# Kernel tuning notes

Measured on AMD Instinct MI355X. Metric: run time of the kernel, lower is better.

## Reference

```python
import jax, jax.numpy as jnp
import numpy as np

NUM_HEADS_SPLIT = 12   # hardcoded in einops reduce pattern
NUM_HEADS_SCALE = 8    # num_heads used only for scale computation (module bug, kept faithful)


def setup_inputs() -> dict:
    key = jax.random.key(0)
    ks = jax.random.split(key, 5)
    B, P, D = 32, 577, 768
    return {
        "x": jax.random.normal(ks[0], (B, P, D), dtype=jnp.float32),
        "qkv_w": jax.random.normal(ks[1], (3 * D, D), dtype=jnp.float32) * 0.02,
        "qkv_b": jax.random.normal(ks[2], (3 * D,), dtype=jnp.float32) * 0.02,
        "out_w": jax.random.normal(ks[3], (D, D), dtype=jnp.float32) * 0.02,
        "out_b": jax.random.normal(ks[4], (D,), dtype=jnp.float32) * 0.02,
    }


def reference(x, qkv_w, qkv_b, out_w, out_b):
    B, P, D = x.shape
    h = NUM_HEADS_SPLIT
    s = D // h
    scale = (D // NUM_HEADS_SCALE) ** -0.5  # 96**-0.5, per original code

    # qkv projection: [B, P, 3D]
    qkv = jnp.einsum('bpd,ed->bpe', x, qkv_w) + qkv_b
    # reshape 'b p (c h s) -> b p c h s' (reduce with mean is a pure reshape here)
    qkv = qkv.reshape(B, P, 3, h, s)
    # split order in the original: v, q, k
    v = jnp.transpose(qkv[:, :, 0], (0, 2, 1, 3))  # [B, h, P, s]
    q = jnp.transpose(qkv[:, :, 1], (0, 2, 1, 3))
    k = jnp.transpose(qkv[:, :, 2], (0, 2, 1, 3))

    attn = jnp.einsum('bhps,bhqs->bhpq', q, k) * scale
    attn = jax.nn.softmax(attn, axis=-1)
    out = jnp.einsum('bhpq,bhqs->bhps', attn, v)  # [B, h, P, s]
    out = jnp.transpose(out, (0, 2, 1, 3)).reshape(B, P, D)

    return jnp.einsum('bpd,ed->bpe', out, out_w) + out_b
```

## Files before the change

### kernel.cpp

```cpp
#include <hip/hip_runtime.h>
#include <stdint.h>

typedef __attribute__((ext_vector_type(8))) short short8;
typedef __attribute__((ext_vector_type(4))) float floatx4;

#define DEV static __device__ __forceinline__

constexpr int Bb = 32, Pp = 577, Dd = 768, Hh = 12;
constexpr int M_VALID = Bb * Pp;
constexpr int M_PAD   = 18560;
constexpr int PKV     = 640;
constexpr float SCALE = 0.10206207261596577f;
constexpr float SCALE_LOG2E = 0.10206207261596577f * 1.4426950408889634f;

DEV ushort f2b(float f) {
  union { float f; uint32_t u; } c; c.f = f;
  uint32_t u = c.u + 0x7fffu + ((c.u >> 16) & 1u);
  return (ushort)(u >> 16);
}

__global__ void cvt_pad(const float* __restrict__ src, ushort* __restrict__ dst,
                        int n_valid4, int n_total4) {
  const float4* s4 = (const float4*)src;
  for (int i = blockIdx.x * blockDim.x + threadIdx.x; i < n_total4;
       i += gridDim.x * blockDim.x) {
    float4 v = make_float4(0.f, 0.f, 0.f, 0.f);
    if (i < n_valid4) v = s4[i];
    ushort4 o;
    o.x = f2b(v.x); o.y = f2b(v.y); o.z = f2b(v.z); o.w = f2b(v.w);
    ((ushort4*)dst)[i] = o;
  }
}

#define STAGE(bi, kk)                                                          \
  do {                                                                         \
    __builtin_amdgcn_global_load_lds(                                          \
        (const __attribute__((address_space(1))) void*)(gA0 + (kk)),           \
        (__attribute__((address_space(3))) void*)(As + (bi)*4096 + tid * 8),   \
        16, 0, 0);                                                             \
    __builtin_amdgcn_global_load_lds(                                          \
        (const __attribute__((address_space(1))) void*)(gA1 + (kk)),           \
        (__attribute__((address_space(3))) void*)(As + (bi)*4096 + 2048 + tid * 8), \
        16, 0, 0);                                                             \
    __builtin_amdgcn_global_load_lds(                                          \
        (const __attribute__((address_space(1))) void*)(gB0 + (kk)),           \
        (__attribute__((address_space(3))) void*)(Bs + (bi)*4096 + tid * 8),   \
        16, 0, 0);                                                             \
    __builtin_amdgcn_global_load_lds(                                          \
        (const __attribute__((address_space(1))) void*)(gB1 + (kk)),           \
        (__attribute__((address_space(3))) void*)(Bs + (bi)*4096 + 2048 + tid * 8), \
        16, 0, 0);                                                             \
  } while (0)

template<bool C_F32>
__global__ __launch_bounds__(256) void gemm_bt(
    const ushort* __restrict__ A, int lda,
    const ushort* __restrict__ Bw,
    const float* __restrict__ bias, void* __restrict__ Cout,
    int N, int K, int m_valid, int nt_n)
{
  __shared__ ushort As[3 * 128 * 32];
  __shared__ ushort Bs[3 * 128 * 32];
  const int tid = threadIdx.x;
  const int lane = tid & 63;
  const int w = tid >> 6;
  const int wr = w >> 1, wc = w & 1;
  const int llo = lane & 15, lhi = lane >> 4;

  const int nwg = gridDim.x;
  const int L = blockIdx.x;
  const int q = nwg >> 3, r = nwg & 7;
  const int xcd = L & 7, pos = L >> 3;
  const int wgid = (xcd < r ? xcd * (q + 1) : r * (q + 1) + (xcd - r) * q) + pos;
  const int m0 = (wgid / nt_n) * 128, n0 = (wgid % nt_n) * 128;

  floatx4 acc[4][4];
#pragma unroll
  for (int i = 0; i < 4; ++i)
#pragma unroll
    for (int j = 0; j < 4; ++j) acc[i][j] = floatx4{0.f, 0.f, 0.f, 0.f};

  const int srow = tid >> 2;
  const int scol = (tid & 3) * 8;
  const ushort* gA0 = A  + (size_t)(m0 + srow) * lda + scol;
  const ushort* gA1 = A  + (size_t)(m0 + 64 + srow) * lda + scol;
  const ushort* gB0 = Bw + (size_t)(n0 + srow) * K + scol;
  const ushort* gB1 = Bw + (size_t)(n0 + 64 + srow) * K + scol;

  STAGE(0, 0);
  STAGE(1, 32);
  int cur = 0;
  for (int kk = 0; kk < K; kk += 32) {
    if (kk + 64 < K) {
      int b2 = cur + 2; if (b2 >= 3) b2 -= 3;
      STAGE(b2, kk + 64);
      asm volatile("s_waitcnt vmcnt(8)" ::: "memory");
    } else if (kk + 32 < K) {
      asm volatile("s_waitcnt vmcnt(4)" ::: "memory");
    } else {
      asm volatile("s_waitcnt vmcnt(0)" ::: "memory");
    }
    __builtin_amdgcn_s_barrier();
    __builtin_amdgcn_sched_barrier(0);

    const ushort* Ab = As + cur * 4096;
    const ushort* Bbp = Bs + cur * 4096;
    short8 af[4], bfr[4];
#pragma unroll
    for (int i = 0; i < 4; ++i) {
      af[i]  = *(const short8*)(Ab + (wr * 64 + i * 16 + llo) * 32 + lhi * 8);
      bfr[i] = *(const short8*)(Bbp + (wc * 64 + i * 16 + llo) * 32 + lhi * 8);
    }
#pragma unroll
    for (int i = 0; i < 4; ++i)
#pragma unroll
      for (int j = 0; j < 4; ++j)
        acc[i][j] = __builtin_amdgcn_mfma_f32_16x16x32_bf16(af[i], bfr[j], acc[i][j], 0, 0, 0);

    __builtin_amdgcn_sched_barrier(0);
    __builtin_amdgcn_s_barrier();
    cur += 1; if (cur >= 3) cur -= 3;
  }

  float bv[4];
#pragma unroll
  for (int j = 0; j < 4; ++j) bv[j] = bias[n0 + wc * 64 + j * 16 + llo];

#pragma unroll
  for (int i = 0; i < 4; ++i) {
#pragma unroll
    for (int r2 = 0; r2 < 4; ++r2) {
      const int row = m0 + wr * 64 + i * 16 + lhi * 4 + r2;
      if (C_F32 && row >= m_valid) continue;
      const size_t rb = (size_t)row * N + n0 + wc * 64;
#pragma unroll
      for (int j = 0; j < 4; ++j) {
        float v = acc[i][j][r2] + bv[j];
        if (C_F32) ((float*)Cout)[rb + j * 16 + llo] = v;
        else       ((ushort*)Cout)[rb + j * 16 + llo] = f2b(v);
      }
    }
  }
}

__global__ __launch_bounds__(256) void vtrans(const ushort* __restrict__ C1,
                                              ushort* __restrict__ Vt) {
  const int pt = blockIdx.x, h = blockIdx.y, b = blockIdx.z;
  __shared__ ushort Ts[64][72];
  const int t = threadIdx.x;
  const int rl = t >> 2, c16 = (t & 3) * 16;
  const int p = pt * 64 + rl;
  short8 a0 = {0,0,0,0,0,0,0,0}, a1 = {0,0,0,0,0,0,0,0};
  if (p < Pp) {
    const ushort* s = C1 + (size_t)(b * Pp + p) * 2304 + h * 64 + c16;
    a0 = *(const short8*)s;
    a1 = *(const short8*)(s + 8);
  }
  *(short8*)&Ts[rl][c16] = a0;
  *(short8*)&Ts[rl][c16 + 8] = a1;
  __syncthreads();
  const int ss = t >> 2, pc16 = (t & 3) * 16;
  short8 o0, o1;
#pragma unroll
  for (int i = 0; i < 8; ++i) {
    o0[i] = (short)Ts[pc16 + i][ss];
    o1[i] = (short)Ts[pc16 + 8 + i][ss];
  }
  ushort* d = Vt + ((size_t)(b * Hh + h) * 64 + ss) * PKV + pt * 64 + pc16;
  *(short8*)d = o0;
  *(short8*)(d + 8) = o1;
}

__global__ __launch_bounds__(512) void attn_fwd(
    ushort* C1, const ushort* __restrict__ Vt)
{
  const int qt = blockIdx.x, h = blockIdx.y, b = blockIdx.z;
  const int tid = threadIdx.x;
  const int lane = tid & 63, w = tid >> 6;
  const int llo = lane & 15, lhi = lane >> 4;

  __shared__ ushort Ks[64][72];
  __shared__ ushort Vs[64][72];
  __shared__ ushort Ps[8][16][72];

  const int q0 = qt * 128;
  const int qrow = q0 + w * 16 + llo;
  const size_t qoff = (size_t)(b * Pp + qrow) * 2304 + 768 + h * 64;
  const short8 qf0 = *(const short8*)(C1 + qoff + lhi * 8);
  const short8 qf1 = *(const short8*)(C1 + qoff + 32 + lhi * 8);

  float ls[4] = {0.f, 0.f, 0.f, 0.f};
  floatx4 acc_o[4];
#pragma unroll
  for (int st = 0; st < 4; ++st) acc_o[st] = floatx4{0.f, 0.f, 0.f, 0.f};

  const int srow = tid >> 3;
  const int sc8 = (tid & 7) * 8;
  const ushort* kbase = C1 + (size_t)(b * Pp + srow) * 2304 + 1536 + h * 64 + sc8;
  const ushort* vbase = Vt + ((size_t)(b * Hh + h) * 64 + srow) * PKV + sc8;

  short8 kc = *(const short8*)(kbase);
  short8 vc = *(const short8*)(vbase);

  for (int t = 0; t < 10; ++t) {
    __syncthreads();
    *(short8*)&Ks[srow][sc8] = kc;
    *(short8*)&Vs[srow][sc8] = vc;
    if (t < 9) {
      kc = *(const short8*)(kbase + (size_t)(t + 1) * 64 * 2304);
      vc = *(const short8*)(vbase + (t + 1) * 64);
    }
    __syncthreads();

    float pv[4][4];
#pragma unroll
    for (int ntl = 0; ntl < 4; ++ntl) {
      floatx4 acc = floatx4{0.f, 0.f, 0.f, 0.f};
      const short8 bf0 = *(const short8*)&Ks[ntl * 16 + llo][lhi * 8];
      const short8 bf1 = *(const short8*)&Ks[ntl * 16 + llo][32 + lhi * 8];
      acc = __builtin_amdgcn_mfma_f32_16x16x32_bf16(qf0, bf0, acc, 0, 0, 0);
      acc = __builtin_amdgcn_mfma_f32_16x16x32_bf16(qf1, bf1, acc, 0, 0, 0);
      const bool valid = (t * 64 + ntl * 16 + llo) < Pp;
#pragma unroll
      for (int r = 0; r < 4; ++r) {
        const float p = valid ? exp2f(acc[r] * SCALE_LOG2E) : 0.f;
        pv[ntl][r] = p;
        ls[r] += p;
      }
    }

#pragma unroll
    for (int r = 0; r < 4; ++r)
#pragma unroll
      for (int ntl = 0; ntl < 4; ++ntl)
        Ps[w][lhi * 4 + r][ntl * 16 + llo] = f2b(pv[ntl][r]);

    const short8 pa0 = *(const short8*)&Ps[w][llo][lhi * 8];
    const short8 pa1 = *(const short8*)&Ps[w][llo][32 + lhi * 8];
#pragma unroll
    for (int st = 0; st < 4; ++st) {
      const short8 vb0 = *(const short8*)&Vs[st * 16 + llo][lhi * 8];
      const short8 vb1 = *(const short8*)&Vs[st * 16 + llo][32 + lhi * 8];
      acc_o[st] = __builtin_amdgcn_mfma_f32_16x16x32_bf16(pa0, vb0, acc_o[st], 0, 0, 0);
      acc_o[st] = __builtin_amdgcn_mfma_f32_16x16x32_bf16(pa1, vb1, acc_o[st], 0, 0, 0);
    }
  }

#pragma unroll
  for (int r = 0; r < 4; ++r) {
#pragma unroll
    for (int off = 1; off < 16; off <<= 1) ls[r] += __shfl_xor(ls[r], off, 64);
  }

#pragma unroll
  for (int r = 0; r < 4; ++r) {
    const int p = q0 + w * 16 + lhi * 4 + r;
    if (p < Pp) {
      const float inv = 1.f / ls[r];
      const size_t ob = (size_t)(b * Pp + p) * 2304 + h * 64;
#pragma unroll
      for (int st = 0; st < 4; ++st)
        C1[ob + st * 16 + llo] = f2b(acc_o[st][r] * inv);
    }
  }
}

extern "C" void kernel_launch(void* const* d_in, const int* in_sizes, int n_in,
                              void* d_out, int out_size, void* d_ws, size_t ws_size,
                              hipStream_t stream) {
  const float* x     = (const float*)d_in[0];
  const float* qkv_w = (const float*)d_in[1];
  const float* qkv_b = (const float*)d_in[2];
  const float* out_w = (const float*)d_in[3];
  const float* out_b = (const float*)d_in[4];
  float* out = (float*)d_out;

  char* ws = (char*)d_ws;
  ushort* C1b = (ushort*)(ws);
  ushort* W3b = (ushort*)(ws + 85524480);
  ushort* W1b = (ushort*)(ws + 86704128);
  ushort* Xb  = (ushort*)(ws + 90243072);
  ushort* Vtb = (ushort*)(ws + 86704128);

  cvt_pad<<<2048, 256, 0, stream>>>(x, Xb, M_VALID * 768 / 4, M_PAD * 768 / 4);
  cvt_pad<<<1024, 256, 0, stream>>>(qkv_w, W1b, 2304 * 768 / 4, 2304 * 768 / 4);
  cvt_pad<<<512, 256, 0, stream>>>(out_w, W3b, 768 * 768 / 4, 768 * 768 / 4);

  gemm_bt<false><<<dim3(145 * 18), 256, 0, stream>>>(Xb, 768, W1b, qkv_b,
                                                     (void*)C1b, 2304, 768, M_PAD, 18);
  vtrans<<<dim3(10, 12, 32), 256, 0, stream>>>(C1b, Vtb);
  attn_fwd<<<dim3(5, 12, 32), 512, 0, stream>>>(C1b, Vtb);
  gemm_bt<true><<<dim3(145 * 6), 256, 0, stream>>>(C1b, 2304, W3b, out_b,
                                                   (void*)out, 768, 768, M_VALID, 6);
}
```

Before: 355.4 us.

## Enlarge GEMM tiles to 256x128 with k-major LDS layout

The GEMM kernel moves from 128x128 to 256x128 output tiles, so each wave computes 128x64 with 32 accumulators. The LDS staging becomes k-chunk-major (each thread loads one A row across four 8-element chunks), which changes the fragment read addressing. It adds a launch_bounds occupancy hint and reorganizes the workspace so the larger padded M range fits. This is meant to raise operand reuse per LDS load and cut global traffic, at the cost of more registers and fewer workgroups (73 row tiles), with a partial last tile that writes are now bounded for.

```diff
diff --git a/kernel.cpp b/kernel.cpp
--- a/kernel.cpp
+++ b/kernel.cpp
@@ -10,7 +10,6 @@
 constexpr int M_VALID = Bb * Pp;
 constexpr int M_PAD   = 18560;
 constexpr int PKV     = 640;
-constexpr float SCALE = 0.10206207261596577f;
 constexpr float SCALE_LOG2E = 0.10206207261596577f * 1.4426950408889634f;
 
 DEV ushort f2b(float f) {
@@ -34,33 +33,29 @@
 
 #define STAGE(bi, kk)                                                          \
   do {                                                                         \
-    __builtin_amdgcn_global_load_lds(                                          \
-        (const __attribute__((address_space(1))) void*)(gA0 + (kk)),           \
-        (__attribute__((address_space(3))) void*)(As + (bi)*4096 + tid * 8),   \
-        16, 0, 0);                                                             \
-    __builtin_amdgcn_global_load_lds(                                          \
-        (const __attribute__((address_space(1))) void*)(gA1 + (kk)),           \
-        (__attribute__((address_space(3))) void*)(As + (bi)*4096 + 2048 + tid * 8), \
-        16, 0, 0);                                                             \
-    __builtin_amdgcn_global_load_lds(                                          \
-        (const __attribute__((address_space(1))) void*)(gB0 + (kk)),           \
-        (__attribute__((address_space(3))) void*)(Bs + (bi)*4096 + tid * 8),   \
-        16, 0, 0);                                                             \
-    __builtin_amdgcn_global_load_lds(                                          \
-        (const __attribute__((address_space(1))) void*)(gB1 + (kk)),           \
-        (__attribute__((address_space(3))) void*)(Bs + (bi)*4096 + 2048 + tid * 8), \
-        16, 0, 0);                                                             \
+    _Pragma("unroll")                                                          \
+    for (int c_ = 0; c_ < 4; ++c_)                                             \
+      __builtin_amdgcn_global_load_lds(                                        \
+          (const __attribute__((address_space(1))) void*)(gA + c_ * 8 + (kk)), \
+          (__attribute__((address_space(3))) void*)(As + (bi)*8192 + c_*2048 + tid*8), \
+          16, 0, 0);                                                           \
+    _Pragma("unroll")                                                          \
+    for (int c_ = 0; c_ < 2; ++c_)                                             \
+      __builtin_amdgcn_global_load_lds(                                        \
+          (const __attribute__((address_space(1))) void*)(gB + c_ * 16 + (kk)),\
+          (__attribute__((address_space(3))) void*)(Bs + (bi)*4096 + c_*2048 + tid*8), \
+          16, 0, 0);                                                           \
   } while (0)
 
 template<bool C_F32>
-__global__ __launch_bounds__(256) void gemm_bt(
+__global__ __launch_bounds__(256, 2) void gemm_bt(
     const ushort* __restrict__ A, int lda,
     const ushort* __restrict__ Bw,
     const float* __restrict__ bias, void* __restrict__ Cout,
     int N, int K, int m_valid, int nt_n)
 {
-  __shared__ ushort As[3 * 128 * 32];
-  __shared__ ushort Bs[3 * 128 * 32];
+  __shared__ ushort As[3 * 8192];
+  __shared__ ushort Bs[3 * 4096];
   const int tid = threadIdx.x;
   const int lane = tid & 63;
   const int w = tid >> 6;
@@ -72,20 +67,16 @@
   const int q = nwg >> 3, r = nwg & 7;
   const int xcd = L & 7, pos = L >> 3;
   const int wgid = (xcd < r ? xcd * (q + 1) : r * (q + 1) + (xcd - r) * q) + pos;
-  const int m0 = (wgid / nt_n) * 128, n0 = (wgid % nt_n) * 128;
-
-  floatx4 acc[4][4];
-#pragma unroll
-  for (int i = 0; i < 4; ++i)
+  const int m0 = (wgid / nt_n) * 256, n0 = (wgid % nt_n) * 128;
+
+  floatx4 acc[8][4];
+#pragma unroll
+  for (int i = 0; i < 8; ++i)
 #pragma unroll
     for (int j = 0; j < 4; ++j) acc[i][j] = floatx4{0.f, 0.f, 0.f, 0.f};
 
-  const int srow = tid >> 2;
-  const int scol = (tid & 3) * 8;
-  const ushort* gA0 = A  + (size_t)(m0 + srow) * lda + scol;
-  const ushort* gA1 = A  + (size_t)(m0 + 64 + srow) * lda + scol;
-  const ushort* gB0 = Bw + (size_t)(n0 + srow) * K + scol;
-  const ushort* gB1 = Bw + (size_t)(n0 + 64 + srow) * K + scol;
+  const ushort* gA = A + ((size_t)m0 + tid) * lda;
+  const ushort* gB = Bw + (size_t)(n0 + (tid & 127)) * K + (tid >> 7) * 8;
 
   STAGE(0, 0);
   STAGE(1, 32);
@@ -94,25 +85,26 @@
     if (kk + 64 < K) {
       int b2 = cur + 2; if (b2 >= 3) b2 -= 3;
       STAGE(b2, kk + 64);
-      asm volatile("s_waitcnt vmcnt(8)" ::: "memory");
+      asm volatile("s_waitcnt vmcnt(12)" ::: "memory");
     } else if (kk + 32 < K) {
-      asm volatile("s_waitcnt vmcnt(4)" ::: "memory");
+      asm volatile("s_waitcnt vmcnt(6)" ::: "memory");
     } else {
       asm volatile("s_waitcnt vmcnt(0)" ::: "memory");
     }
     __builtin_amdgcn_s_barrier();
     __builtin_amdgcn_sched_barrier(0);
 
-    const ushort* Ab = As + cur * 4096;
+    const ushort* Ab = As + cur * 8192;
     const ushort* Bbp = Bs + cur * 4096;
-    short8 af[4], bfr[4];
-#pragma unroll
-    for (int i = 0; i < 4; ++i) {
-      af[i]  = *(const short8*)(Ab + (wr * 64 + i * 16 + llo) * 32 + lhi * 8);
-      bfr[i] = *(const short8*)(Bbp + (wc * 64 + i * 16 + llo) * 32 + lhi * 8);
-    }
-#pragma unroll
-    for (int i = 0; i < 4; ++i)
+    short8 af[8], bfr[4];
+#pragma unroll
+    for (int j = 0; j < 4; ++j)
+      bfr[j] = *(const short8*)(Bbp + lhi * 1024 + (wc * 64 + j * 16 + llo) * 8);
+#pragma unroll
+    for (int i = 0; i < 8; ++i)
+      af[i] = *(const short8*)(Ab + lhi * 2048 + (wr * 128 + i * 16 + llo) * 8);
+#pragma unroll
+    for (int i = 0; i < 8; ++i)
 #pragma unroll
       for (int j = 0; j < 4; ++j)
         acc[i][j] = __builtin_amdgcn_mfma_f32_16x16x32_bf16(af[i], bfr[j], acc[i][j], 0, 0, 0);
@@ -127,11 +119,11 @@
   for (int j = 0; j < 4; ++j) bv[j] = bias[n0 + wc * 64 + j * 16 + llo];
 
 #pragma unroll
-  for (int i = 0; i < 4; ++i) {
+  for (int i = 0; i < 8; ++i) {
 #pragma unroll
     for (int r2 = 0; r2 < 4; ++r2) {
-      const int row = m0 + wr * 64 + i * 16 + lhi * 4 + r2;
-      if (C_F32 && row >= m_valid) continue;
+      const int row = m0 + wr * 128 + i * 16 + lhi * 4 + r2;
+      if (row >= m_valid) continue;
       const size_t rb = (size_t)row * N + n0 + wc * 64;
 #pragma unroll
       for (int j = 0; j < 4; ++j) {
@@ -276,20 +268,20 @@
   float* out = (float*)d_out;
 
   char* ws = (char*)d_ws;
-  ushort* C1b = (ushort*)(ws);
-  ushort* W3b = (ushort*)(ws + 85524480);
-  ushort* W1b = (ushort*)(ws + 86704128);
-  ushort* Xb  = (ushort*)(ws + 90243072);
-  ushort* Vtb = (ushort*)(ws + 86704128);
+  ushort* Xb  = (ushort*)(ws);
+  ushort* W1b = (ushort*)(ws + 28508160);
+  ushort* C1b = (ushort*)(ws + 32047104);
+  ushort* W3b = (ushort*)(ws + 117571584);
+  ushort* Vtb = (ushort*)(ws);
 
   cvt_pad<<<2048, 256, 0, stream>>>(x, Xb, M_VALID * 768 / 4, M_PAD * 768 / 4);
   cvt_pad<<<1024, 256, 0, stream>>>(qkv_w, W1b, 2304 * 768 / 4, 2304 * 768 / 4);
   cvt_pad<<<512, 256, 0, stream>>>(out_w, W3b, 768 * 768 / 4, 768 * 768 / 4);
 
-  gemm_bt<false><<<dim3(145 * 18), 256, 0, stream>>>(Xb, 768, W1b, qkv_b,
-                                                     (void*)C1b, 2304, 768, M_PAD, 18);
+  gemm_bt<false><<<dim3(73 * 18), 256, 0, stream>>>(Xb, 768, W1b, qkv_b,
+                                                    (void*)C1b, 2304, 768, M_PAD, 18);
   vtrans<<<dim3(10, 12, 32), 256, 0, stream>>>(C1b, Vtb);
   attn_fwd<<<dim3(5, 12, 32), 512, 0, stream>>>(C1b, Vtb);
-  gemm_bt<true><<<dim3(145 * 6), 256, 0, stream>>>(C1b, 2304, W3b, out_b,
-                                                   (void*)out, 768, 768, M_VALID, 6);
-}
+  gemm_bt<true><<<dim3(73 * 6), 256, 0, stream>>>(C1b, 2304, W3b, out_b,
+                                                  (void*)out, 768, 768, M_VALID, 6);
+}
```

New measurement: 417.1 us. 17.4% more time.
